# Kernel tuning notes

Measured on AMD Instinct MI355X. Metric: run time of the kernel, lower is better.

The kernel has to match this reference:

```python
import jax, jax.numpy as jnp
import numpy as np

NUM_HEADS = 8
WINDOW_SIZE = 4
DIM = 384


def setup_inputs() -> dict:
    key = jax.random.key(0)
    k_x, k_qkv, k_pw, k_pb = jax.random.split(key, 4)
    B, N, C = 8, 16384, DIM
    x = jax.random.normal(k_x, (B, N, C), dtype=jnp.float32)
    # torch nn.Linear weights are [out_features, in_features]
    W_qkv = jax.random.normal(k_qkv, (3 * C, C), dtype=jnp.float32) * (1.0 / np.sqrt(C))
    W_proj = jax.random.normal(k_pw, (C, C), dtype=jnp.float32) * (1.0 / np.sqrt(C))
    b_proj = jax.random.normal(k_pb, (C,), dtype=jnp.float32) * 0.01
    return {"x": x, "W_qkv": W_qkv, "W_proj": W_proj, "b_proj": b_proj}


def reference(x, W_qkv, W_proj, b_proj):
    B, N, C = x.shape
    H = int(round(N ** 0.5))
    W = H
    ws = WINDOW_SIZE
    nh = NUM_HEADS
    hd = C // nh
    scale = hd ** -0.5
    hw, ww = H // ws, W // ws

    qkv = x @ W_qkv.T  # [B, N, 3C]
    qkv = qkv.reshape(B, N, 3, nh, hd)
    qkv = jnp.transpose(qkv, (2, 0, 3, 1, 4))  # [3, B, nh, N, hd]
    q, k, v = qkv[0], qkv[1], qkv[2]

    def to_windows(t):
        # [B, nh, N, hd] -> [B, nh, n_windows, ws*ws, hd]
        t = t.reshape(B, nh, hw, ws, ww, ws, hd)
        t = jnp.transpose(t, (0, 1, 2, 4, 3, 5, 6))
        return t.reshape(B, nh, hw * ww, ws * ws, hd)

    q, k, v = to_windows(q), to_windows(k), to_windows(v)

    attn = jnp.einsum('bhwqd,bhwkd->bhwqk', q, k) * scale
    attn = jax.nn.softmax(attn, axis=-1)
    out = jnp.einsum('bhwqk,bhwkd->bhwqd', attn, v)

    # windows back to [B, N, C]
    out = out.reshape(B, nh, hw, ww, ws, ws, hd)
    out = jnp.transpose(out, (0, 1, 2, 4, 3, 5, 6)).reshape(B, nh, N, hd)
    out = jnp.transpose(out, (0, 2, 1, 3)).reshape(B, N, C)

    out = out @ W_proj.T + b_proj
    return out
```

## Files before the change

### kernel.cpp

```cpp
#include <hip/hip_runtime.h>
#include <hip/hip_bf16.h>
#include <cstdint>

#define ASPACE(n) __attribute__((address_space(n)))

typedef short bf16x8 __attribute__((ext_vector_type(8)));
typedef float f32x4 __attribute__((ext_vector_type(4)));

__device__ __forceinline__ unsigned short f2bf(float f) {
  uint32_t u = __float_as_uint(f);
  u += 0x7fffu + ((u >> 16) & 1u);
  return (unsigned short)(u >> 16);
}
__device__ __forceinline__ float bf2f(unsigned short h) {
  return __uint_as_float(((uint32_t)h) << 16);
}

__device__ __forceinline__ bf16x8 cvt8(float4 a, float4 b) {
  union { uint32_t u[4]; bf16x8 v; } r;
  asm("v_cvt_pk_bf16_f32 %0, %1, %2" : "=v"(r.u[0]) : "v"(a.x), "v"(a.y));
  asm("v_cvt_pk_bf16_f32 %0, %1, %2" : "=v"(r.u[1]) : "v"(a.z), "v"(a.w));
  asm("v_cvt_pk_bf16_f32 %0, %1, %2" : "=v"(r.u[2]) : "v"(b.x), "v"(b.y));
  asm("v_cvt_pk_bf16_f32 %0, %1, %2" : "=v"(r.u[3]) : "v"(b.z), "v"(b.w));
  return r.v;
}

__global__ __launch_bounds__(256) void conv_f32_bf16(const float4* __restrict__ src,
                                                     ushort4* __restrict__ dst, int n4) {
  int i = blockIdx.x * blockDim.x + threadIdx.x;
  int stride = gridDim.x * blockDim.x;
  for (; i < n4; i += stride) {
    float4 v = src[i];
    ushort4 o;
    o.x = f2bf(v.x); o.y = f2bf(v.y); o.z = f2bf(v.z); o.w = f2bf(v.w);
    dst[i] = o;
  }
}

__device__ __forceinline__ void gload16(const unsigned short* g, unsigned short* l) {
  __builtin_amdgcn_global_load_lds((const ASPACE(1) void*)g, (ASPACE(3) void*)l, 16, 0, 0);
}

__global__ __launch_bounds__(256, 3) void gemm_qkv(const float* __restrict__ x,
                                                   const unsigned short* __restrict__ B,
                                                   unsigned short* __restrict__ C,
                                                   int M, int N, int K) {
  __shared__ unsigned short As[2][128 * 32];
  __shared__ unsigned short Bs[2][192 * 32];

  const int tid  = threadIdx.x;
  const int lane = tid & 63;
  const int wave = tid >> 6;
  const int wr = wave >> 1;
  const int wc = wave & 1;

  const int nwg = gridDim.x;
  const int swz = (blockIdx.x & 7) * (nwg >> 3) + (blockIdx.x >> 3);
  const int ntn = N / 192;
  const int bn0 = (swz % ntn) * 192;
  const int bm0 = (swz / ntn) << 7;

  const unsigned short* Bbase = B + (size_t)bn0 * K;

  const float* gAf[2];
  int wAo[2];
#pragma unroll
  for (int i = 0; i < 2; ++i) {
    const int c = i * 256 + tid;
    const int r = c >> 2;
    const int gc = (c & 3) ^ ((r >> 1) & 3);
    gAf[i] = x + (size_t)(bm0 + r) * K + gc * 8;
    wAo[i] = c * 8;
  }
  const unsigned short* gB[3];
  unsigned short* lB[3];
#pragma unroll
  for (int i = 0; i < 3; ++i) {
    const int c = i * 256 + tid;
    const int r = c >> 2;
    const int gc = (c & 3) ^ ((r >> 1) & 3);
    gB[i] = Bbase + (size_t)r * K + gc * 8;
    lB[i] = (unsigned short*)Bs + (i * 256 + wave * 64) * 8;
  }
  const int abufoff = 128 * 32;
  const int bbufoff = 192 * 32;

  const int fr = lane & 15;
  const int hi = lane >> 4;
  int afo[4], bfo[6];
#pragma unroll
  for (int m = 0; m < 4; ++m) {
    const int row = wr * 64 + m * 16 + fr;
    afo[m] = row * 32 + ((hi ^ ((row >> 1) & 3)) * 8);
  }
#pragma unroll
  for (int n = 0; n < 6; ++n) {
    const int row = wc * 96 + n * 16 + fr;
    bfo[n] = row * 32 + ((hi ^ ((row >> 1) & 3)) * 8);
  }

  f32x4 acc[4][6];
#pragma unroll
  for (int m = 0; m < 4; ++m)
#pragma unroll
    for (int n = 0; n < 6; ++n) {
      f32x4 z = {0.f, 0.f, 0.f, 0.f};
      acc[m][n] = z;
    }

  const int NT = K >> 5;

  float4 a0[2], a1[2];
#pragma unroll
  for (int i = 0; i < 2; ++i) { a0[i] = *(const float4*)(gAf[i]); a1[i] = *(const float4*)(gAf[i] + 4); }
#pragma unroll
  for (int i = 0; i < 3; ++i) gload16(gB[i], lB[i]);
#pragma unroll
  for (int i = 0; i < 2; ++i)
    *(bf16x8*)((unsigned short*)As + wAo[i]) = cvt8(a0[i], a1[i]);
  __syncthreads();

  int cur = 0;
  for (int t = 0; t < NT; ++t) {
    const int nb = cur ^ 1;
    if (t + 1 < NT) {
      const int k0 = (t + 1) << 5;
#pragma unroll
      for (int i = 0; i < 2; ++i) { a0[i] = *(const float4*)(gAf[i] + k0); a1[i] = *(const float4*)(gAf[i] + k0 + 4); }
#pragma unroll
      for (int i = 0; i < 3; ++i) gload16(gB[i] + k0, lB[i] + nb * bbufoff);
    }
    {
      const unsigned short* Ab = (const unsigned short*)As + cur * abufoff;
      const unsigned short* Bb = (const unsigned short*)Bs + cur * bbufoff;
      bf16x8 af[4], bfv[6];
#pragma unroll
      for (int m = 0; m < 4; ++m) af[m] = *(const bf16x8*)(Ab + afo[m]);
#pragma unroll
      for (int n = 0; n < 6; ++n) bfv[n] = *(const bf16x8*)(Bb + bfo[n]);
#pragma unroll
      for (int m = 0; m < 4; ++m)
#pragma unroll
        for (int n = 0; n < 6; ++n)
          acc[m][n] = __builtin_amdgcn_mfma_f32_16x16x32_bf16(af[m], bfv[n], acc[m][n], 0, 0, 0);
    }
    if (t + 1 < NT) {
#pragma unroll
      for (int i = 0; i < 2; ++i)
        *(bf16x8*)((unsigned short*)As + nb * abufoff + wAo[i]) = cvt8(a0[i], a1[i]);
    }
    __syncthreads();
    cur ^= 1;
  }

  const int rq = hi * 4;
#pragma unroll
  for (int m = 0; m < 4; ++m) {
#pragma unroll
    for (int n = 0; n < 6; ++n) {
      const int col = bn0 + wc * 96 + n * 16 + fr;
      const int pl = col / 48;
      const int d  = col - pl * 48;
      unsigned short* base = C + ((size_t)pl * M + bm0 + wr * 64 + m * 16 + rq) * 48 + d;
#pragma unroll
      for (int r = 0; r < 4; ++r)
        base[(size_t)r * 48] = f2bf(acc[m][n][r]);
    }
  }
}

#define MTOK 131072
#define ASTR 392
__global__ __launch_bounds__(512, 2) void fused_attn_proj(const unsigned short* __restrict__ qkv,
                                                          const unsigned short* __restrict__ Wp,
                                                          const float* __restrict__ bias,
                                                          float* __restrict__ out) {
  __shared__ unsigned short lds[50176 + 24576];
  unsigned short* attn = lds;
  unsigned short* BsS  = lds + 50176;

  const int tid = threadIdx.x, lane = tid & 63, wave = tid >> 6;
  const int nwg = gridDim.x;
  const int swz = (blockIdx.x & 7) * (nwg >> 3) + (blockIdx.x >> 3);
  const int b = swz >> 7, g2 = swz & 127;
  const int yb = g2 >> 2, xb = g2 & 3;
  const int imgbase = b * 16384;

  const int lg = lane >> 4;
  const int lr = lane & 15;

  {
    unsigned short* Vt = BsS + wave * 1536;
    unsigned short* P  = Vt + 48 * 24;
    const int gtok = imgbase + (yb * 4 + (lr >> 2)) * 128 + xb * 32 + wave * 4 + (lr & 3);

    for (int h = 0; h < 8; ++h) {
      const size_t qb = ((size_t)h * MTOK + gtok) * 48;
      const size_t kb = ((size_t)(8 + h) * MTOK + gtok) * 48;
      const size_t vb = ((size_t)(16 + h) * MTOK + gtok) * 48;

      bf16x8 aq0 = *(const bf16x8*)(qkv + qb + lg * 8);
      bf16x8 bk0 = *(const bf16x8*)(qkv + kb + lg * 8);
      bf16x8 aq1 = {0, 0, 0, 0, 0, 0, 0, 0};
      bf16x8 bk1 = {0, 0, 0, 0, 0, 0, 0, 0};
      if (lg < 2) {
        aq1 = *(const bf16x8*)(qkv + qb + 32 + lg * 8);
        bk1 = *(const bf16x8*)(qkv + kb + 32 + lg * 8);
      }
      {
        bf16x8 v = *(const bf16x8*)(qkv + vb + lg * 8);
#pragma unroll
        for (int i = 0; i < 8; ++i) Vt[(lg * 8 + i) * 24 + lr] = (unsigned short)v[i];
        if (lane < 32) {
          bf16x8 v2 = *(const bf16x8*)(qkv + vb + 32 + lg * 8);
#pragma unroll
          for (int i = 0; i < 8; ++i) Vt[((4 + lg) * 8 + i) * 24 + lr] = (unsigned short)v2[i];
        }
      }

      f32x4 s = {0.f, 0.f, 0.f, 0.f};
      s = __builtin_amdgcn_mfma_f32_16x16x32_bf16(aq0, bk0, s, 0, 0, 0);
      s = __builtin_amdgcn_mfma_f32_16x16x32_bf16(aq1, bk1, s, 0, 0, 0);

      const float scale = 0.14433756729740643f;
      float p[4];
#pragma unroll
      for (int r = 0; r < 4; ++r) {
        float xv = s[r] * scale;
        float m = xv;
        m = fmaxf(m, __shfl_xor(m, 1));
        m = fmaxf(m, __shfl_xor(m, 2));
        m = fmaxf(m, __shfl_xor(m, 4));
        m = fmaxf(m, __shfl_xor(m, 8));
        float e = __expf(xv - m);
        float tt = e;
        tt += __shfl_xor(tt, 1);
        tt += __shfl_xor(tt, 2);
        tt += __shfl_xor(tt, 4);
        tt += __shfl_xor(tt, 8);
        p[r] = e / tt;
      }
#pragma unroll
      for (int r = 0; r < 4; ++r) P[(lg * 4 + r) * 24 + lr] = f2bf(p[r]);

      bf16x8 ap = {0, 0, 0, 0, 0, 0, 0, 0};
      if (lg < 2) ap = *(const bf16x8*)(P + lr * 24 + lg * 8);

      f32x4 o[3];
#pragma unroll
      for (int c = 0; c < 3; ++c) {
        bf16x8 bv = {0, 0, 0, 0, 0, 0, 0, 0};
        if (lg < 2) bv = *(const bf16x8*)(Vt + (c * 16 + lr) * 24 + lg * 8);
        f32x4 z = {0.f, 0.f, 0.f, 0.f};
        o[c] = __builtin_amdgcn_mfma_f32_16x16x32_bf16(ap, bv, z, 0, 0, 0);
      }

#pragma unroll
      for (int r = 0; r < 4; ++r) {
        const int qi = lg * 4 + r;
        const int lq = (qi >> 2) * 32 + wave * 4 + (qi & 3);
#pragma unroll
        for (int c = 0; c < 3; ++c)
          attn[lq * ASTR + h * 48 + c * 16 + lr] = f2bf(o[c][r]);
      }
    }
  }
  __syncthreads();

  const int fr = lane & 15;
  const int hi = lane >> 4;
  const int wr = wave >> 1;
  const int wc = wave & 1;

  const unsigned short* gB[3];
  unsigned short* lB[3];
#pragma unroll
  for (int i = 0; i < 3; ++i) {
    const int c = i * 512 + tid;
    const int r = c >> 2;
    const int gc = (c & 3) ^ ((r >> 1) & 3);
    gB[i] = Wp + (size_t)r * 384 + gc * 8;
    lB[i] = BsS + (i * 512 + wave * 64) * 8;
  }
  const int bbufoff = 384 * 32;

  int afo[2], bfo[12];
#pragma unroll
  for (int mf = 0; mf < 2; ++mf) {
    const int row = wr * 32 + mf * 16 + fr;
    afo[mf] = row * ASTR;
  }
#pragma unroll
  for (int nf = 0; nf < 12; ++nf) {
    const int row = wc * 192 + nf * 16 + fr;
    bfo[nf] = row * 32 + ((hi ^ ((row >> 1) & 3)) * 8);
  }

  f32x4 acc[2][12];
#pragma unroll
  for (int mf = 0; mf < 2; ++mf)
#pragma unroll
    for (int nf = 0; nf < 12; ++nf) {
      f32x4 z = {0.f, 0.f, 0.f, 0.f};
      acc[mf][nf] = z;
    }

#pragma unroll
  for (int i = 0; i < 3; ++i) gload16(gB[i], lB[i]);
  __syncthreads();

  int cur = 0;
  for (int t = 0; t < 12; ++t) {
    if (t + 1 < 12) {
      const int nb = cur ^ 1;
      const int k0 = (t + 1) << 5;
#pragma unroll
      for (int i = 0; i < 3; ++i) gload16(gB[i] + k0, lB[i] + nb * bbufoff);
    }
    {
      const unsigned short* Bb = BsS + cur * bbufoff;
      bf16x8 af[2], bfv[12];
#pragma unroll
      for (int mf = 0; mf < 2; ++mf)
        af[mf] = *(const bf16x8*)(attn + afo[mf] + t * 32 + hi * 8);
#pragma unroll
      for (int nf = 0; nf < 12; ++nf) bfv[nf] = *(const bf16x8*)(Bb + bfo[nf]);
#pragma unroll
      for (int mf = 0; mf < 2; ++mf)
#pragma unroll
        for (int nf = 0; nf < 12; ++nf)
          acc[mf][nf] = __builtin_amdgcn_mfma_f32_16x16x32_bf16(af[mf], bfv[nf], acc[mf][nf], 0, 0, 0);
    }
    __syncthreads();
    cur ^= 1;
  }

  const int rq = hi * 4;
#pragma unroll
  for (int mf = 0; mf < 2; ++mf) {
#pragma unroll
    for (int nf = 0; nf < 12; ++nf) {
      const int col = wc * 192 + nf * 16 + fr;
      const float bv = bias[col];
#pragma unroll
      for (int r = 0; r < 4; ++r) {
        const int l = wr * 32 + mf * 16 + rq + r;
        const int gtok = imgbase + (yb * 4 + (l >> 5)) * 128 + xb * 32 + (l & 31);
        out[(size_t)gtok * 384 + col] = acc[mf][nf][r] + bv;
      }
    }
  }
}

extern "C" void kernel_launch(void* const* d_in, const int* in_sizes, int n_in,
                              void* d_out, int out_size, void* d_ws, size_t ws_size,
                              hipStream_t stream) {
  const float* x      = (const float*)d_in[0];
  const float* W_qkv  = (const float*)d_in[1];
  const float* W_proj = (const float*)d_in[2];
  const float* b_proj = (const float*)d_in[3];
  float* out = (float*)d_out;

  const int Bb = 8, Nn = 16384, Cc = 384;
  const int M = Bb * Nn;
  const int threeC = 3 * Cc;

  char* ws = (char*)d_ws;
  unsigned short* qkv_bf   = (unsigned short*)ws;
  unsigned short* wqkv_bf  = (unsigned short*)(ws + (size_t)M * threeC * 2);
  unsigned short* wproj_bf = wqkv_bf + threeC * Cc;

  conv_f32_bf16<<<432, 256, 0, stream>>>((const float4*)W_qkv, (ushort4*)wqkv_bf,
                                         threeC * Cc / 4);
  conv_f32_bf16<<<144, 256, 0, stream>>>((const float4*)W_proj, (ushort4*)wproj_bf,
                                         Cc * Cc / 4);

  gemm_qkv<<<(M / 128) * (threeC / 192), 256, 0, stream>>>(x, wqkv_bf, qkv_bf,
                                                           M, threeC, Cc);

  fused_attn_proj<<<M / 128, 512, 0, stream>>>(qkv_bf, wproj_bf, b_proj, out);
}
```

Baseline: 387.1 us.

## Prefetch A tiles two stages ahead with manual waitcnt and hardcoded K

Hardcodes K=384 so the k-loop fully unrolls into 12 iterations. The fp32 A-tile global loads are issued two iterations ahead in registers, while the B tile goes to LDS one iteration ahead. __syncthreads is replaced by explicit s_waitcnt vmcnt(4) plus s_barrier and sched_barriers, so the next A loads stay in flight across the barrier. This hides global load latency in the QKV GEMM at the cost of extra registers, and it ignores the K argument.

```diff
diff --git a/kernel.cpp b/kernel.cpp
--- a/kernel.cpp
+++ b/kernel.cpp
@@ -44,7 +44,8 @@
 __global__ __launch_bounds__(256, 3) void gemm_qkv(const float* __restrict__ x,
                                                    const unsigned short* __restrict__ B,
                                                    unsigned short* __restrict__ C,
-                                                   int M, int N, int K) {
+                                                   int M, int N, int K_unused) {
+  const int K = 384;
   __shared__ unsigned short As[2][128 * 32];
   __shared__ unsigned short Bs[2][192 * 32];
 
@@ -108,28 +109,40 @@
       acc[m][n] = z;
     }
 
-  const int NT = K >> 5;
-
-  float4 a0[2], a1[2];
-#pragma unroll
-  for (int i = 0; i < 2; ++i) { a0[i] = *(const float4*)(gAf[i]); a1[i] = *(const float4*)(gAf[i] + 4); }
+  float4 p0a, p0b, p1a, p1b, q0a, q0b, q1a, q1b;
+
+  p0a = *(const float4*)(gAf[0]);     p0b = *(const float4*)(gAf[0] + 4);
+  p1a = *(const float4*)(gAf[1]);     p1b = *(const float4*)(gAf[1] + 4);
+  __builtin_amdgcn_sched_barrier(0);
 #pragma unroll
   for (int i = 0; i < 3; ++i) gload16(gB[i], lB[i]);
-#pragma unroll
-  for (int i = 0; i < 2; ++i)
-    *(bf16x8*)((unsigned short*)As + wAo[i]) = cvt8(a0[i], a1[i]);
-  __syncthreads();
-
-  int cur = 0;
-  for (int t = 0; t < NT; ++t) {
-    const int nb = cur ^ 1;
-    if (t + 1 < NT) {
+  __builtin_amdgcn_sched_barrier(0);
+  q0a = *(const float4*)(gAf[0] + 32); q0b = *(const float4*)(gAf[0] + 36);
+  q1a = *(const float4*)(gAf[1] + 32); q1b = *(const float4*)(gAf[1] + 36);
+  __builtin_amdgcn_sched_barrier(0);
+  *(bf16x8*)((unsigned short*)As + wAo[0]) = cvt8(p0a, p0b);
+  *(bf16x8*)((unsigned short*)As + wAo[1]) = cvt8(p1a, p1b);
+  asm volatile("s_waitcnt vmcnt(4) lgkmcnt(0)" ::: "memory");
+  __builtin_amdgcn_s_barrier();
+  __builtin_amdgcn_sched_barrier(0);
+  p0a = q0a; p0b = q0b; p1a = q1a; p1b = q1b;
+
+#pragma unroll
+  for (int t = 0; t < 12; ++t) {
+    const int cur = t & 1;
+    const int nb  = cur ^ 1;
+    if (t < 11) {
       const int k0 = (t + 1) << 5;
 #pragma unroll
-      for (int i = 0; i < 2; ++i) { a0[i] = *(const float4*)(gAf[i] + k0); a1[i] = *(const float4*)(gAf[i] + k0 + 4); }
-#pragma unroll
       for (int i = 0; i < 3; ++i) gload16(gB[i] + k0, lB[i] + nb * bbufoff);
     }
+    __builtin_amdgcn_sched_barrier(0);
+    if (t < 10) {
+      const int k0 = (t + 2) << 5;
+      q0a = *(const float4*)(gAf[0] + k0); q0b = *(const float4*)(gAf[0] + k0 + 4);
+      q1a = *(const float4*)(gAf[1] + k0); q1b = *(const float4*)(gAf[1] + k0 + 4);
+    }
+    __builtin_amdgcn_sched_barrier(0);
     {
       const unsigned short* Ab = (const unsigned short*)As + cur * abufoff;
       const unsigned short* Bb = (const unsigned short*)Bs + cur * bbufoff;
@@ -144,13 +157,18 @@
         for (int n = 0; n < 6; ++n)
           acc[m][n] = __builtin_amdgcn_mfma_f32_16x16x32_bf16(af[m], bfv[n], acc[m][n], 0, 0, 0);
     }
-    if (t + 1 < NT) {
-#pragma unroll
-      for (int i = 0; i < 2; ++i)
-        *(bf16x8*)((unsigned short*)As + nb * abufoff + wAo[i]) = cvt8(a0[i], a1[i]);
-    }
-    __syncthreads();
-    cur ^= 1;
+    if (t < 11) {
+      *(bf16x8*)((unsigned short*)As + nb * abufoff + wAo[0]) = cvt8(p0a, p0b);
+      *(bf16x8*)((unsigned short*)As + nb * abufoff + wAo[1]) = cvt8(p1a, p1b);
+      if (t < 10) {
+        asm volatile("s_waitcnt vmcnt(4) lgkmcnt(0)" ::: "memory");
+      } else {
+        asm volatile("s_waitcnt vmcnt(0) lgkmcnt(0)" ::: "memory");
+      }
+      __builtin_amdgcn_s_barrier();
+      __builtin_amdgcn_sched_barrier(0);
+      p0a = q0a; p0b = q0b; p1a = q1a; p1b = q1b;
+    }
   }
 
   const int rq = hi * 4;
```

Measured after the change: 475.8 us. 22.9% more time.
